# Kernel optimization log

Measured on AMD Instinct MI355X. Metric: run time of the kernel, lower is better.

## Reference

```python
import jax, jax.numpy as jnp
import numpy as np

B, S, H, HID, V, NSPEC = 8, 4096, 1024, 128, 60000, 5
EPS = 1e-12
SLOPE = 0.01  # nn.LeakyReLU default negative_slope


def _leaky(x):
    return jnp.where(x >= 0, x, SLOPE * x)


def setup_inputs() -> dict:
    key = jax.random.key(0)
    ks = jax.random.split(key, 12)
    gene_ids = jax.random.randint(ks[0], (B, S), 0, V)
    cont = jax.random.uniform(ks[1], (B, S), jnp.float32, 0.0, 10.0)
    spec_mask = jax.random.uniform(ks[2], (B, S)) < 0.05
    spec_vals = -jax.random.randint(ks[3], (B, S), 1, NSPEC + 1).astype(jnp.float32)
    expr_values = jnp.where(spec_mask, spec_vals, cont)
    gene_emb = jax.random.normal(ks[4], (V, H), jnp.float32) * 0.02
    W1 = jax.random.normal(ks[5], (HID,), jnp.float32) * 0.5   # Linear(1,128) weight
    b1 = jax.random.normal(ks[6], (HID,), jnp.float32) * 0.1
    W2 = jax.random.normal(ks[7], (HID, H), jnp.float32) * 0.05  # Linear(128,H)
    b2 = jax.random.normal(ks[8], (H,), jnp.float32) * 0.1
    special_emb = jax.random.normal(ks[9], (NSPEC, HID), jnp.float32) * 0.02
    special_emb = special_emb.at[2].set(0.0)  # padding_idx=2
    pos_emb = jax.random.normal(ks[10], (S, H), jnp.float32) * 0.02
    gamma = jnp.ones((H,), jnp.float32)
    beta = jnp.zeros((H,), jnp.float32)
    return dict(gene_ids=gene_ids, expr_values=expr_values, gene_emb=gene_emb,
                W1=W1, b1=b1, W2=W2, b2=b2, special_emb=special_emb,
                pos_emb=pos_emb, gamma=gamma, beta=beta)


def reference(gene_ids, expr_values, gene_emb, W1, b1, W2, b2, special_emb,
              pos_emb, gamma, beta):
    x = expr_values                                  # [B,S]
    special = x < 0                                  # special-token mask
    # mapped special id: -(int(x)+1); clamp so gather is in-range on non-special slots
    mapped = jnp.clip(-(x.astype(jnp.int32) + 1), 0, NSPEC - 1)
    spec_e = special_emb[mapped]                     # [B,S,HID] gather
    cont_e = _leaky(x[..., None] * W1 + b1)          # dense_1 on scalar value
    h = jnp.where(special[..., None], spec_e, cont_e)  # scatter-combine
    expr_e = _leaky(h) @ W2 + b2                     # dense_2 -> [B,S,H]
    emb = gene_emb[gene_ids] + expr_e + pos_emb[None, :, :]
    mu = jnp.mean(emb, axis=-1, keepdims=True)
    var = jnp.mean(jnp.square(emb - mu), axis=-1, keepdims=True)
    out = (emb - mu) * jax.lax.rsqrt(var + EPS) * gamma + beta
    return out  # dropout is identity at inference (p used at train only)
```

## Files before the change

kernel.cpp:

```cpp
#include <hip/hip_runtime.h>
#include <hip/hip_bf16.h>

#define B_DIM   8
#define S_LEN   4096
#define H_DIM   1024
#define HID_DIM 128
#define NSPEC   5
#define NROWS   (HID_DIM + 1 + NSPEC)
#define SLOPE   0.01f
#define LN_EPS  1e-12f

typedef float vfloat4 __attribute__((ext_vector_type(4)));

__global__ __launch_bounds__(256) void build_kernel(
        const float* __restrict__ W1,
        const float* __restrict__ b1,
        const float* __restrict__ W2,
        const float* __restrict__ b2,
        const float* __restrict__ spec,
        float* __restrict__ tvals,
        float2* __restrict__ tab) {
    const int row = blockIdx.x;
    const int tid = threadIdx.x;

    __shared__ float tsh[HID_DIM];
    __shared__ float ash[HID_DIM];
    __shared__ float csh[HID_DIM];

    float w = 0.0f, b = 0.0f, t = 0.0f;
    if (tid < HID_DIM) {
        w = W1[tid];
        b = b1[tid];
        t = (w != 0.0f) ? (-b / w) : __builtin_inff();
        tsh[tid] = t;
        if (row == 0) tvals[tid] = t;
    }
    __syncthreads();
    if (tid < HID_DIM) {
        int r = 0;
        #pragma unroll 8
        for (int k2 = 0; k2 < HID_DIM; ++k2) {
            const float t2 = tsh[k2];
            if (t2 < t || (t2 == t && k2 < tid)) ++r;
        }

        float a, c;
        if (row <= HID_DIM) {
            const bool crossed = (r < row);
            bool zpos;
            if (w > 0.0f)      zpos = crossed;
            else if (w < 0.0f) zpos = !crossed;
            else               zpos = (b >= 0.0f);
            const float s = zpos ? 1.0f : (SLOPE * SLOPE);
            a = s * w;
            c = s * b;
        } else {
            const int m = row - (HID_DIM + 1);
            const float e = spec[m * HID_DIM + tid];
            a = 0.0f;
            c = (e >= 0.0f) ? e : SLOPE * e;
        }
        ash[tid] = a;
        csh[tid] = c;
    }
    __syncthreads();

    float4 u = make_float4(0.f, 0.f, 0.f, 0.f);
    float4 v = make_float4(0.f, 0.f, 0.f, 0.f);
    #pragma unroll 4
    for (int k = 0; k < HID_DIM; ++k) {
        const float4 w2 = reinterpret_cast<const float4*>(W2 + (size_t)k * H_DIM)[tid];
        const float a = ash[k], c = csh[k];
        u.x = fmaf(a, w2.x, u.x);  v.x = fmaf(c, w2.x, v.x);
        u.y = fmaf(a, w2.y, u.y);  v.y = fmaf(c, w2.y, v.y);
        u.z = fmaf(a, w2.z, u.z);  v.z = fmaf(c, w2.z, v.z);
        u.w = fmaf(a, w2.w, u.w);  v.w = fmaf(c, w2.w, v.w);
    }
    const float4 bb = reinterpret_cast<const float4*>(b2)[tid];
    float4* trow = reinterpret_cast<float4*>(tab + (size_t)row * H_DIM);
    trow[2 * tid]     = make_float4(u.x, v.x + bb.x, u.y, v.y + bb.y);
    trow[2 * tid + 1] = make_float4(u.z, v.z + bb.z, u.w, v.w + bb.w);
}

__global__ __launch_bounds__(256) void fuse_kernel(
        const int*   __restrict__ gene_ids,
        const float* __restrict__ expr,
        const float* __restrict__ gene_emb,
        const float* __restrict__ pos_emb,
        const float* __restrict__ gamma,
        const float* __restrict__ beta,
        const float* __restrict__ tvals,
        const float2* __restrict__ tab,
        float* __restrict__ out) {
    const int tid  = threadIdx.x;
    const int lane = tid & 63;
    const int wv   = tid >> 6;
    const int t0   = blockIdx.x * 8 + wv * 2;
    const int t1   = t0 + 1;
    const int sp0  = t0 & (S_LEN - 1);
    const int sp1  = t1 & (S_LEN - 1);

    const float x0   = expr[t0];
    const float x1   = expr[t1];
    const int   gid0 = gene_ids[t0];
    const int   gid1 = gene_ids[t1];
    const float tka  = tvals[lane];
    const float tkb  = tvals[lane + 64];

    const float4* gp0 = reinterpret_cast<const float4*>(gene_emb + (size_t)gid0 * H_DIM);
    const float4* gp1 = reinterpret_cast<const float4*>(gene_emb + (size_t)gid1 * H_DIM);
    const float4* pp0 = reinterpret_cast<const float4*>(pos_emb  + (size_t)sp0  * H_DIM);
    const float4* pp1 = reinterpret_cast<const float4*>(pos_emb  + (size_t)sp1  * H_DIM);

    float4 g0[4], g1[4], p0[4], p1[4];
    #pragma unroll
    for (int q = 0; q < 4; ++q) {
        const int f = lane + 64 * q;
        g0[q] = gp0[f];
        g1[q] = gp1[f];
        p0[q] = pp0[f];
        p1[q] = pp1[f];
    }

    const int rc0 = __popcll(__ballot(tka <= x0)) + __popcll(__ballot(tkb <= x0));
    const int rc1 = __popcll(__ballot(tka <= x1)) + __popcll(__ballot(tkb <= x1));

    const bool sp_0 = (x0 < 0.0f);
    const bool sp_1 = (x1 < 0.0f);
    int m0 = min(max(-((int)x0) - 1, 0), NSPEC - 1);
    int m1 = min(max(-((int)x1) - 1, 0), NSPEC - 1);
    const int   row0 = sp_0 ? (HID_DIM + 1 + m0) : rc0;
    const int   row1 = sp_1 ? (HID_DIM + 1 + m1) : rc1;
    const float xm0  = sp_0 ? 0.0f : x0;
    const float xm1  = sp_1 ? 0.0f : x1;

    const float4* tp0 = reinterpret_cast<const float4*>(tab + (size_t)row0 * H_DIM);
    const float4* tp1 = reinterpret_cast<const float4*>(tab + (size_t)row1 * H_DIM);
    float4 a0[4], b0[4], a1[4], b1v[4];
    #pragma unroll
    for (int q = 0; q < 4; ++q) {
        const int f = lane + 64 * q;
        a0[q]  = tp0[2 * f];
        b0[q]  = tp0[2 * f + 1];
        a1[q]  = tp1[2 * f];
        b1v[q] = tp1[2 * f + 1];
    }

    float4 gm[4], bt[4];
    #pragma unroll
    for (int q = 0; q < 4; ++q) {
        const int f = lane + 64 * q;
        gm[q] = reinterpret_cast<const float4*>(gamma)[f];
        bt[q] = reinterpret_cast<const float4*>(beta)[f];
    }

    float4 e0[4], e1[4];
    float s1_0 = 0.0f, s2_0 = 0.0f, s1_1 = 0.0f, s2_1 = 0.0f;
    #pragma unroll
    for (int q = 0; q < 4; ++q) {
        float4 ev;
        ev.x = g0[q].x + fmaf(xm0, a0[q].x, a0[q].y) + p0[q].x;
        ev.y = g0[q].y + fmaf(xm0, a0[q].z, a0[q].w) + p0[q].y;
        ev.z = g0[q].z + fmaf(xm0, b0[q].x, b0[q].y) + p0[q].z;
        ev.w = g0[q].w + fmaf(xm0, b0[q].z, b0[q].w) + p0[q].w;
        e0[q] = ev;
        s1_0 += ev.x + ev.y + ev.z + ev.w;
        s2_0 += ev.x * ev.x + ev.y * ev.y + ev.z * ev.z + ev.w * ev.w;

        float4 fv;
        fv.x = g1[q].x + fmaf(xm1, a1[q].x, a1[q].y) + p1[q].x;
        fv.y = g1[q].y + fmaf(xm1, a1[q].z, a1[q].w) + p1[q].y;
        fv.z = g1[q].z + fmaf(xm1, b1v[q].x, b1v[q].y) + p1[q].z;
        fv.w = g1[q].w + fmaf(xm1, b1v[q].z, b1v[q].w) + p1[q].w;
        e1[q] = fv;
        s1_1 += fv.x + fv.y + fv.z + fv.w;
        s2_1 += fv.x * fv.x + fv.y * fv.y + fv.z * fv.z + fv.w * fv.w;
    }

    #pragma unroll
    for (int off = 32; off >= 1; off >>= 1) {
        s1_0 += __shfl_xor(s1_0, off, 64);
        s2_0 += __shfl_xor(s2_0, off, 64);
        s1_1 += __shfl_xor(s1_1, off, 64);
        s2_1 += __shfl_xor(s2_1, off, 64);
    }

    const float inv   = 1.0f / (float)H_DIM;
    const float mu0   = s1_0 * inv;
    const float var0  = s2_0 * inv - mu0 * mu0;
    const float rs0   = rsqrtf(var0 + LN_EPS);
    const float mu1   = s1_1 * inv;
    const float var1  = s2_1 * inv - mu1 * mu1;
    const float rs1   = rsqrtf(var1 + LN_EPS);

    vfloat4* op0 = reinterpret_cast<vfloat4*>(out + (size_t)t0 * H_DIM);
    vfloat4* op1 = reinterpret_cast<vfloat4*>(out + (size_t)t1 * H_DIM);
    #pragma unroll
    for (int q = 0; q < 4; ++q) {
        const int f = lane + 64 * q;
        vfloat4 o;
        o.x = fmaf((e0[q].x - mu0) * rs0, gm[q].x, bt[q].x);
        o.y = fmaf((e0[q].y - mu0) * rs0, gm[q].y, bt[q].y);
        o.z = fmaf((e0[q].z - mu0) * rs0, gm[q].z, bt[q].z);
        o.w = fmaf((e0[q].w - mu0) * rs0, gm[q].w, bt[q].w);
        __builtin_nontemporal_store(o, op0 + f);
        vfloat4 o2;
        o2.x = fmaf((e1[q].x - mu1) * rs1, gm[q].x, bt[q].x);
        o2.y = fmaf((e1[q].y - mu1) * rs1, gm[q].y, bt[q].y);
        o2.z = fmaf((e1[q].z - mu1) * rs1, gm[q].z, bt[q].z);
        o2.w = fmaf((e1[q].w - mu1) * rs1, gm[q].w, bt[q].w);
        __builtin_nontemporal_store(o2, op1 + f);
    }
}

extern "C" void kernel_launch(void* const* d_in, const int* in_sizes, int n_in,
                              void* d_out, int out_size, void* d_ws, size_t ws_size,
                              hipStream_t stream) {
    const int*   gene_ids = (const int*)  d_in[0];
    const float* expr     = (const float*)d_in[1];
    const float* gene_emb = (const float*)d_in[2];
    const float* W1       = (const float*)d_in[3];
    const float* b1       = (const float*)d_in[4];
    const float* W2       = (const float*)d_in[5];
    const float* b2       = (const float*)d_in[6];
    const float* spec     = (const float*)d_in[7];
    const float* pos_emb  = (const float*)d_in[8];
    const float* gamma    = (const float*)d_in[9];
    const float* beta     = (const float*)d_in[10];
    float* out = (float*)d_out;

    const size_t tab_bytes = (size_t)NROWS * H_DIM * sizeof(float2);
    float2* tab   = (float2*)d_ws;
    float*  tvals = (float*)((char*)d_ws + tab_bytes);

    const int n_tokens = in_sizes[0];

    build_kernel<<<NROWS, 256, 0, stream>>>(W1, b1, W2, b2, spec, tvals, tab);
    fuse_kernel<<<n_tokens / 8, 256, 0, stream>>>(gene_ids, expr, gene_emb, pos_emb,
                                                  gamma, beta, tvals, tab, out);
}
```

Before: 74.00 us.

## Use persistent grid-stride fuse kernel with software-prefetched next token pair

Replaces the one-block-per-8-tokens launch with a fixed grid of 512 persistent blocks. Each wave loops over token pairs and issues the gene, position and table row loads for the next pair before finishing the LayerNorm and stores of the current pair. The aim is to hide gather latency and cut block launch overhead. In exchange it roughly doubles live registers (hence launch_bounds 256,2), and the fixed grid may under-fill the GPU or lower occupancy.

```diff
diff --git a/kernel.cpp b/kernel.cpp
--- a/kernel.cpp
+++ b/kernel.cpp
@@ -9,6 +9,7 @@
 #define NROWS   (HID_DIM + 1 + NSPEC)
 #define SLOPE   0.01f
 #define LN_EPS  1e-12f
+#define FUSE_BLOCKS 512
 
 typedef float vfloat4 __attribute__((ext_vector_type(4)));
 
@@ -82,7 +83,7 @@
     trow[2 * tid + 1] = make_float4(u.z, v.z + bb.z, u.w, v.w + bb.w);
 }
 
-__global__ __launch_bounds__(256) void fuse_kernel(
+__global__ __launch_bounds__(256, 2) void fuse_kernel(
         const int*   __restrict__ gene_ids,
         const float* __restrict__ expr,
         const float* __restrict__ gene_emb,
@@ -91,61 +92,16 @@
         const float* __restrict__ beta,
         const float* __restrict__ tvals,
         const float2* __restrict__ tab,
-        float* __restrict__ out) {
-    const int tid  = threadIdx.x;
-    const int lane = tid & 63;
-    const int wv   = tid >> 6;
-    const int t0   = blockIdx.x * 8 + wv * 2;
-    const int t1   = t0 + 1;
-    const int sp0  = t0 & (S_LEN - 1);
-    const int sp1  = t1 & (S_LEN - 1);
-
-    const float x0   = expr[t0];
-    const float x1   = expr[t1];
-    const int   gid0 = gene_ids[t0];
-    const int   gid1 = gene_ids[t1];
-    const float tka  = tvals[lane];
-    const float tkb  = tvals[lane + 64];
-
-    const float4* gp0 = reinterpret_cast<const float4*>(gene_emb + (size_t)gid0 * H_DIM);
-    const float4* gp1 = reinterpret_cast<const float4*>(gene_emb + (size_t)gid1 * H_DIM);
-    const float4* pp0 = reinterpret_cast<const float4*>(pos_emb  + (size_t)sp0  * H_DIM);
-    const float4* pp1 = reinterpret_cast<const float4*>(pos_emb  + (size_t)sp1  * H_DIM);
-
-    float4 g0[4], g1[4], p0[4], p1[4];
-    #pragma unroll
-    for (int q = 0; q < 4; ++q) {
-        const int f = lane + 64 * q;
-        g0[q] = gp0[f];
-        g1[q] = gp1[f];
-        p0[q] = pp0[f];
-        p1[q] = pp1[f];
-    }
-
-    const int rc0 = __popcll(__ballot(tka <= x0)) + __popcll(__ballot(tkb <= x0));
-    const int rc1 = __popcll(__ballot(tka <= x1)) + __popcll(__ballot(tkb <= x1));
-
-    const bool sp_0 = (x0 < 0.0f);
-    const bool sp_1 = (x1 < 0.0f);
-    int m0 = min(max(-((int)x0) - 1, 0), NSPEC - 1);
-    int m1 = min(max(-((int)x1) - 1, 0), NSPEC - 1);
-    const int   row0 = sp_0 ? (HID_DIM + 1 + m0) : rc0;
-    const int   row1 = sp_1 ? (HID_DIM + 1 + m1) : rc1;
-    const float xm0  = sp_0 ? 0.0f : x0;
-    const float xm1  = sp_1 ? 0.0f : x1;
-
-    const float4* tp0 = reinterpret_cast<const float4*>(tab + (size_t)row0 * H_DIM);
-    const float4* tp1 = reinterpret_cast<const float4*>(tab + (size_t)row1 * H_DIM);
-    float4 a0[4], b0[4], a1[4], b1v[4];
-    #pragma unroll
-    for (int q = 0; q < 4; ++q) {
-        const int f = lane + 64 * q;
-        a0[q]  = tp0[2 * f];
-        b0[q]  = tp0[2 * f + 1];
-        a1[q]  = tp1[2 * f];
-        b1v[q] = tp1[2 * f + 1];
-    }
-
+        float* __restrict__ out,
+        int npairs) {
+    const int lane = threadIdx.x & 63;
+    const int wv   = threadIdx.x >> 6;
+    const int NW   = gridDim.x * 4;
+    int pr = blockIdx.x * 4 + wv;
+    if (pr >= npairs) return;
+
+    const float tka = tvals[lane];
+    const float tkb = tvals[lane + 64];
     float4 gm[4], bt[4];
     #pragma unroll
     for (int q = 0; q < 4; ++q) {
@@ -154,62 +110,157 @@
         bt[q] = reinterpret_cast<const float4*>(beta)[f];
     }
 
-    float4 e0[4], e1[4];
-    float s1_0 = 0.0f, s2_0 = 0.0f, s1_1 = 0.0f, s2_1 = 0.0f;
-    #pragma unroll
-    for (int q = 0; q < 4; ++q) {
-        float4 ev;
-        ev.x = g0[q].x + fmaf(xm0, a0[q].x, a0[q].y) + p0[q].x;
-        ev.y = g0[q].y + fmaf(xm0, a0[q].z, a0[q].w) + p0[q].y;
-        ev.z = g0[q].z + fmaf(xm0, b0[q].x, b0[q].y) + p0[q].z;
-        ev.w = g0[q].w + fmaf(xm0, b0[q].z, b0[q].w) + p0[q].w;
-        e0[q] = ev;
-        s1_0 += ev.x + ev.y + ev.z + ev.w;
-        s2_0 += ev.x * ev.x + ev.y * ev.y + ev.z * ev.z + ev.w * ev.w;
-
-        float4 fv;
-        fv.x = g1[q].x + fmaf(xm1, a1[q].x, a1[q].y) + p1[q].x;
-        fv.y = g1[q].y + fmaf(xm1, a1[q].z, a1[q].w) + p1[q].y;
-        fv.z = g1[q].z + fmaf(xm1, b1v[q].x, b1v[q].y) + p1[q].z;
-        fv.w = g1[q].w + fmaf(xm1, b1v[q].z, b1v[q].w) + p1[q].w;
-        e1[q] = fv;
-        s1_1 += fv.x + fv.y + fv.z + fv.w;
-        s2_1 += fv.x * fv.x + fv.y * fv.y + fv.z * fv.z + fv.w * fv.w;
-    }
-
-    #pragma unroll
-    for (int off = 32; off >= 1; off >>= 1) {
-        s1_0 += __shfl_xor(s1_0, off, 64);
-        s2_0 += __shfl_xor(s2_0, off, 64);
-        s1_1 += __shfl_xor(s1_1, off, 64);
-        s2_1 += __shfl_xor(s2_1, off, 64);
-    }
-
-    const float inv   = 1.0f / (float)H_DIM;
-    const float mu0   = s1_0 * inv;
-    const float var0  = s2_0 * inv - mu0 * mu0;
-    const float rs0   = rsqrtf(var0 + LN_EPS);
-    const float mu1   = s1_1 * inv;
-    const float var1  = s2_1 * inv - mu1 * mu1;
-    const float rs1   = rsqrtf(var1 + LN_EPS);
-
-    vfloat4* op0 = reinterpret_cast<vfloat4*>(out + (size_t)t0 * H_DIM);
-    vfloat4* op1 = reinterpret_cast<vfloat4*>(out + (size_t)t1 * H_DIM);
-    #pragma unroll
-    for (int q = 0; q < 4; ++q) {
-        const int f = lane + 64 * q;
-        vfloat4 o;
-        o.x = fmaf((e0[q].x - mu0) * rs0, gm[q].x, bt[q].x);
-        o.y = fmaf((e0[q].y - mu0) * rs0, gm[q].y, bt[q].y);
-        o.z = fmaf((e0[q].z - mu0) * rs0, gm[q].z, bt[q].z);
-        o.w = fmaf((e0[q].w - mu0) * rs0, gm[q].w, bt[q].w);
-        __builtin_nontemporal_store(o, op0 + f);
-        vfloat4 o2;
-        o2.x = fmaf((e1[q].x - mu1) * rs1, gm[q].x, bt[q].x);
-        o2.y = fmaf((e1[q].y - mu1) * rs1, gm[q].y, bt[q].y);
-        o2.z = fmaf((e1[q].z - mu1) * rs1, gm[q].z, bt[q].z);
-        o2.w = fmaf((e1[q].w - mu1) * rs1, gm[q].w, bt[q].w);
-        __builtin_nontemporal_store(o2, op1 + f);
+    float x0 = expr[2 * pr];
+    float x1 = expr[2 * pr + 1];
+    int gid0 = gene_ids[2 * pr];
+    int gid1 = gene_ids[2 * pr + 1];
+
+    float xm0, xm1;
+    {
+        const int rc0 = __popcll(__ballot(tka <= x0)) + __popcll(__ballot(tkb <= x0));
+        const int rc1 = __popcll(__ballot(tka <= x1)) + __popcll(__ballot(tkb <= x1));
+        const bool sA = (x0 < 0.0f), sB = (x1 < 0.0f);
+        const int mA = min(max(-((int)x0) - 1, 0), NSPEC - 1);
+        const int mB = min(max(-((int)x1) - 1, 0), NSPEC - 1);
+        gid0 = gid0;
+        xm0 = sA ? 0.0f : x0;
+        xm1 = sB ? 0.0f : x1;
+        const int row0 = sA ? (HID_DIM + 1 + mA) : rc0;
+        const int row1 = sB ? (HID_DIM + 1 + mB) : rc1;
+        x0 = __int_as_float(row0);
+        x1 = __int_as_float(row1);
+    }
+    int row0 = __float_as_int(x0);
+    int row1 = __float_as_int(x1);
+
+    float4 g0[4], g1[4], p0[4], p1[4], a0[4], b0[4], a1[4], b1v[4];
+    {
+        const int sp0 = (2 * pr) & (S_LEN - 1);
+        const float4* gp0 = reinterpret_cast<const float4*>(gene_emb + (size_t)gid0 * H_DIM);
+        const float4* gp1 = reinterpret_cast<const float4*>(gene_emb + (size_t)gid1 * H_DIM);
+        const float4* pp0 = reinterpret_cast<const float4*>(pos_emb  + (size_t)sp0  * H_DIM);
+        const float4* pp1 = pp0 + (H_DIM / 4);
+        const float4* tp0 = reinterpret_cast<const float4*>(tab + (size_t)row0 * H_DIM);
+        const float4* tp1 = reinterpret_cast<const float4*>(tab + (size_t)row1 * H_DIM);
+        #pragma unroll
+        for (int q = 0; q < 4; ++q) {
+            const int f = lane + 64 * q;
+            g0[q]  = gp0[f];
+            g1[q]  = gp1[f];
+            p0[q]  = pp0[f];
+            p1[q]  = pp1[f];
+            a0[q]  = tp0[2 * f];
+            b0[q]  = tp0[2 * f + 1];
+            a1[q]  = tp1[2 * f];
+            b1v[q] = tp1[2 * f + 1];
+        }
+    }
+
+    for (;;) {
+        const int pn   = pr + NW;
+        const bool more = (pn < npairs);
+
+        float nx0 = 0.0f, nx1 = 0.0f;
+        int  ng0 = 0, ng1 = 0;
+        if (more) {
+            nx0 = expr[2 * pn];
+            nx1 = expr[2 * pn + 1];
+            ng0 = gene_ids[2 * pn];
+            ng1 = gene_ids[2 * pn + 1];
+        }
+
+        float4 e0[4], e1[4];
+        float s1_0 = 0.0f, s2_0 = 0.0f, s1_1 = 0.0f, s2_1 = 0.0f;
+        #pragma unroll
+        for (int q = 0; q < 4; ++q) {
+            float4 ev;
+            ev.x = g0[q].x + fmaf(xm0, a0[q].x, a0[q].y) + p0[q].x;
+            ev.y = g0[q].y + fmaf(xm0, a0[q].z, a0[q].w) + p0[q].y;
+            ev.z = g0[q].z + fmaf(xm0, b0[q].x, b0[q].y) + p0[q].z;
+            ev.w = g0[q].w + fmaf(xm0, b0[q].z, b0[q].w) + p0[q].w;
+            e0[q] = ev;
+            s1_0 += ev.x + ev.y + ev.z + ev.w;
+            s2_0 += ev.x * ev.x + ev.y * ev.y + ev.z * ev.z + ev.w * ev.w;
+
+            float4 fv;
+            fv.x = g1[q].x + fmaf(xm1, a1[q].x, a1[q].y) + p1[q].x;
+            fv.y = g1[q].y + fmaf(xm1, a1[q].z, a1[q].w) + p1[q].y;
+            fv.z = g1[q].z + fmaf(xm1, b1v[q].x, b1v[q].y) + p1[q].z;
+            fv.w = g1[q].w + fmaf(xm1, b1v[q].z, b1v[q].w) + p1[q].w;
+            e1[q] = fv;
+            s1_1 += fv.x + fv.y + fv.z + fv.w;
+            s2_1 += fv.x * fv.x + fv.y * fv.y + fv.z * fv.z + fv.w * fv.w;
+        }
+
+        float nxm0 = 0.0f, nxm1 = 0.0f;
+        if (more) {
+            const int rc0 = __popcll(__ballot(tka <= nx0)) + __popcll(__ballot(tkb <= nx0));
+            const int rc1 = __popcll(__ballot(tka <= nx1)) + __popcll(__ballot(tkb <= nx1));
+            const bool sA = (nx0 < 0.0f), sB = (nx1 < 0.0f);
+            const int mA = min(max(-((int)nx0) - 1, 0), NSPEC - 1);
+            const int mB = min(max(-((int)nx1) - 1, 0), NSPEC - 1);
+            const int nrow0 = sA ? (HID_DIM + 1 + mA) : rc0;
+            const int nrow1 = sB ? (HID_DIM + 1 + mB) : rc1;
+            nxm0 = sA ? 0.0f : nx0;
+            nxm1 = sB ? 0.0f : nx1;
+
+            const int sp0 = (2 * pn) & (S_LEN - 1);
+            const float4* gp0 = reinterpret_cast<const float4*>(gene_emb + (size_t)ng0 * H_DIM);
+            const float4* gp1 = reinterpret_cast<const float4*>(gene_emb + (size_t)ng1 * H_DIM);
+            const float4* pp0 = reinterpret_cast<const float4*>(pos_emb  + (size_t)sp0 * H_DIM);
+            const float4* pp1 = pp0 + (H_DIM / 4);
+            const float4* tp0 = reinterpret_cast<const float4*>(tab + (size_t)nrow0 * H_DIM);
+            const float4* tp1 = reinterpret_cast<const float4*>(tab + (size_t)nrow1 * H_DIM);
+            #pragma unroll
+            for (int q = 0; q < 4; ++q) {
+                const int f = lane + 64 * q;
+                g0[q]  = gp0[f];
+                g1[q]  = gp1[f];
+                p0[q]  = pp0[f];
+                p1[q]  = pp1[f];
+                a0[q]  = tp0[2 * f];
+                b0[q]  = tp0[2 * f + 1];
+                a1[q]  = tp1[2 * f];
+                b1v[q] = tp1[2 * f + 1];
+            }
+        }
+
+        #pragma unroll
+        for (int off = 32; off >= 1; off >>= 1) {
+            s1_0 += __shfl_xor(s1_0, off, 64);
+            s2_0 += __shfl_xor(s2_0, off, 64);
+            s1_1 += __shfl_xor(s1_1, off, 64);
+            s2_1 += __shfl_xor(s2_1, off, 64);
+        }
+        const float inv  = 1.0f / (float)H_DIM;
+        const float mu0  = s1_0 * inv;
+        const float rs0  = rsqrtf(s2_0 * inv - mu0 * mu0 + LN_EPS);
+        const float mu1  = s1_1 * inv;
+        const float rs1  = rsqrtf(s2_1 * inv - mu1 * mu1 + LN_EPS);
+
+        vfloat4* op0 = reinterpret_cast<vfloat4*>(out + (size_t)(2 * pr) * H_DIM);
+        vfloat4* op1 = op0 + (H_DIM / 4);
+        #pragma unroll
+        for (int q = 0; q < 4; ++q) {
+            const int f = lane + 64 * q;
+            vfloat4 o;
+            o.x = fmaf((e0[q].x - mu0) * rs0, gm[q].x, bt[q].x);
+            o.y = fmaf((e0[q].y - mu0) * rs0, gm[q].y, bt[q].y);
+            o.z = fmaf((e0[q].z - mu0) * rs0, gm[q].z, bt[q].z);
+            o.w = fmaf((e0[q].w - mu0) * rs0, gm[q].w, bt[q].w);
+            __builtin_nontemporal_store(o, op0 + f);
+            vfloat4 o2;
+            o2.x = fmaf((e1[q].x - mu1) * rs1, gm[q].x, bt[q].x);
+            o2.y = fmaf((e1[q].y - mu1) * rs1, gm[q].y, bt[q].y);
+            o2.z = fmaf((e1[q].z - mu1) * rs1, gm[q].z, bt[q].z);
+            o2.w = fmaf((e1[q].w - mu1) * rs1, gm[q].w, bt[q].w);
+            __builtin_nontemporal_store(o2, op1 + f);
+        }
+
+        if (!more) break;
+        pr  = pn;
+        xm0 = nxm0;
+        xm1 = nxm1;
     }
 }
 
@@ -234,8 +285,9 @@
     float*  tvals = (float*)((char*)d_ws + tab_bytes);
 
     const int n_tokens = in_sizes[0];
+    const int npairs   = n_tokens / 2;
 
     build_kernel<<<NROWS, 256, 0, stream>>>(W1, b1, W2, b2, spec, tvals, tab);
-    fuse_kernel<<<n_tokens / 8, 256, 0, stream>>>(gene_ids, expr, gene_emb, pos_emb,
-                                                  gamma, beta, tvals, tab, out);
+    fuse_kernel<<<FUSE_BLOCKS, 256, 0, stream>>>(gene_ids, expr, gene_emb, pos_emb,
+                                                 gamma, beta, tvals, tab, out, npairs);
 }
```

Result: slower. 159.6 us (+115.7%).
